# Optimization experiments

Hardware: AMD Instinct MI355X
Metric: run time of the kernel (lower is better)

Reference implementation:

```python
import jax, jax.numpy as jnp
import numpy as np

NUM_GRAPHS = 256
N_NODES = 100000
N_EDGES = 1200000
NODE_DIM = 64
NUM_LAYERS = 3
R_HID = 128
R_OUT = 32


def setup_inputs() -> dict:
    key = jax.random.key(0)
    ks = jax.random.split(key, 10)
    x = jax.random.normal(ks[0], (N_NODES, NODE_DIM), dtype=jnp.float32)
    src = jax.random.randint(ks[1], (N_EDGES,), 0, N_NODES)
    dst = jax.random.randint(ks[2], (N_EDGES,), 0, N_NODES)
    graph_ids = jnp.sort(jax.random.randint(ks[3], (N_NODES,), 0, NUM_GRAPHS))
    s = 1.0 / np.sqrt(NODE_DIM)
    gin_W = jax.random.normal(ks[4], (NUM_LAYERS, NODE_DIM, NODE_DIM), dtype=jnp.float32) * s
    gin_b = jnp.zeros((NUM_LAYERS, NODE_DIM), dtype=jnp.float32)
    eps = jnp.zeros((NUM_LAYERS,), dtype=jnp.float32)  # learnable GIN epsilon
    in_dim = NODE_DIM * NUM_LAYERS
    r_W1 = jax.random.normal(ks[5], (in_dim, R_HID), dtype=jnp.float32) / np.sqrt(in_dim)
    r_b1 = jnp.zeros((R_HID,), dtype=jnp.float32)
    r_W2 = jax.random.normal(ks[6], (R_HID, R_OUT), dtype=jnp.float32) / np.sqrt(R_HID)
    r_b2 = jnp.zeros((R_OUT,), dtype=jnp.float32)
    return {"x": x, "gin_W": gin_W, "gin_b": gin_b, "eps": eps,
            "r_W1": r_W1, "r_b1": r_b1, "r_W2": r_W2, "r_b2": r_b2,
            "src": src, "dst": dst, "graph_ids": graph_ids}


def reference(x, gin_W, gin_b, eps, r_W1, r_b1, r_W2, r_b2, src, dst, graph_ids):
    n = x.shape[0]
    h = x
    hs = []
    for l in range(NUM_LAYERS):  # fixed small layer loop
        # neighbor sum aggregation: scatter-add messages h[src] into dst
        agg = jax.ops.segment_sum(h[src], dst, num_segments=n)  # [N, D]
        h = jax.nn.relu(((1.0 + eps[l]) * h + agg) @ gin_W[l] + gin_b[l])
        hs.append(h)
    H = jnp.stack(hs, axis=1)  # [N, L, D]
    # dgl.sum_nodes per layer output == ragged segment-sum over graph ids
    g = jax.ops.segment_sum(H, graph_ids, num_segments=NUM_GRAPHS)  # [B, L, D]
    g = g.reshape(NUM_GRAPHS, -1)  # [B, L*D]
    # readout MLP (2 layers)
    out = jax.nn.relu(g @ r_W1 + r_b1) @ r_W2 + r_b2
    return out
```

## Files before the change

kernel.cpp:

```cpp
#include <hip/hip_runtime.h>


#define SPLIT 16
#define NBLK 512
#define BS 512

typedef unsigned short ushort_t;
typedef __bf16 v8bf __attribute__((ext_vector_type(8)));
typedef float v4f __attribute__((ext_vector_type(4)));

__device__ __forceinline__ float h2f_lo(unsigned int v) {
    return (float)__builtin_bit_cast(_Float16, (unsigned short)(v & 0xffffu));
}
__device__ __forceinline__ float h2f_hi(unsigned int v) {
    return (float)__builtin_bit_cast(_Float16, (unsigned short)(v >> 16));
}
__device__ __forceinline__ unsigned int f2h(float f) {
    return (unsigned int)__builtin_bit_cast(unsigned short, (_Float16)f);
}

__global__ __launch_bounds__(256) void pre_kernel(
        const int* __restrict__ dst, int* __restrict__ cnt2d,
        int E, int nbkt, int ebpb,
        const float* __restrict__ x, ushort_t* __restrict__ xh, int n4, int castBlocks,
        const float* __restrict__ W, ushort_t* __restrict__ whi,
        ushort_t* __restrict__ wlo, int wtotal) {
    __shared__ int lcnt[256];
    int t = threadIdx.x;
    int blk = blockIdx.x;
    if (blk < NBLK) {
        lcnt[t] = 0;
        __syncthreads();
        int base = blk * ebpb;
        int end = min(base + ebpb, E);
        for (int i = base + t; i < end; i += 256)
            atomicAdd(&lcnt[dst[i] >> 9], 1);
        __syncthreads();
        if (t < nbkt) cnt2d[(size_t)blk * nbkt + t] = lcnt[t];
    } else if (blk < NBLK + castBlocks) {
        int i = (blk - NBLK) * 256 + t;
        if (i < n4) {
            float4 v = ((const float4*)x)[i];
            uint2 p;
            p.x = f2h(v.x) | (f2h(v.y) << 16);
            p.y = f2h(v.z) | (f2h(v.w) << 16);
            ((uint2*)xh)[i] = p;
        }
    } else {
        int i = (blk - NBLK - castBlocks) * 256 + t;
        if (i < wtotal) {
            int l = i >> 12, r = i & 4095;
            int n = r >> 6, k = r & 63;
            float w = W[l * 4096 + k * 64 + n];
            __bf16 h = (__bf16)w;
            float rem = w - (float)h;
            whi[i] = __builtin_bit_cast(ushort_t, h);
            wlo[i] = __builtin_bit_cast(ushort_t, (__bf16)rem);
        }
    }
}

__global__ __launch_bounds__(256) void colscan_kernel(
        const int* __restrict__ cnt2d, int* __restrict__ blkoff,
        int* __restrict__ btot, int nbkt) {
    __shared__ int sh[256];
    int b = blockIdx.x, t = threadIdx.x;
    int i0 = 2 * t, i1 = 2 * t + 1;
    int v0 = cnt2d[(size_t)i0 * nbkt + b];
    int v1 = cnt2d[(size_t)i1 * nbkt + b];
    int pair = v0 + v1;
    sh[t] = pair;
    __syncthreads();
    for (int off = 1; off < 256; off <<= 1) {
        int u = (t >= off) ? sh[t - off] : 0;
        __syncthreads();
        sh[t] += u;
        __syncthreads();
    }
    int ex = sh[t] - pair;
    blkoff[(size_t)b * NBLK + i0] = ex;
    blkoff[(size_t)b * NBLK + i1] = ex + v0;
    if (t == 255) btot[b] = sh[255];
}

__global__ __launch_bounds__(256) void bucket_base_kernel(
        const int* __restrict__ btot, int* __restrict__ bbase,
        int* __restrict__ offsets, int nbkt, int N, int E) {
    __shared__ int sh[256];
    int t = threadIdx.x;
    int v = (t < nbkt) ? btot[t] : 0;
    sh[t] = v;
    __syncthreads();
    for (int off = 1; off < 256; off <<= 1) {
        int u = (t >= off) ? sh[t - off] : 0;
        __syncthreads();
        sh[t] += u;
        __syncthreads();
    }
    if (t < nbkt) bbase[t] = sh[t] - v;
    if (t == 0) { bbase[nbkt] = E; offsets[N] = E; }
}

__global__ __launch_bounds__(256) void bucket_scatter_kernel(
        const int* __restrict__ src, const int* __restrict__ dst,
        const int* __restrict__ bbase, const int* __restrict__ blkoff,
        unsigned int* __restrict__ bkt, int E, int nbkt, int ebpb) {
    __shared__ int lbase[256];
    __shared__ int lrank[256];
    int t = threadIdx.x;
    if (t < nbkt) lbase[t] = bbase[t] + blkoff[(size_t)t * NBLK + blockIdx.x];
    lrank[t] = 0;
    __syncthreads();
    int base = blockIdx.x * ebpb;
    int end = min(base + ebpb, E);
    for (int i = base + t; i < end; i += 256) {
        int d = dst[i];
        int b = d >> 9;
        int r = atomicAdd(&lrank[b], 1);
        bkt[lbase[b] + r] = ((unsigned int)src[i] << 9) | (unsigned int)(d & (BS - 1));
    }
}

__global__ __launch_bounds__(256) void csr_build_kernel(
        const unsigned int* __restrict__ bkt, const int* __restrict__ bbase,
        int* __restrict__ offsets, int* __restrict__ csr, int N, int nbkt) {
    __shared__ int cnt[BS];
    __shared__ int rank[BS];
    __shared__ int sh[256];
    int b = blockIdx.x, t = threadIdx.x;
    cnt[t] = 0; cnt[t + 256] = 0;
    rank[t] = 0; rank[t + 256] = 0;
    __syncthreads();
    int base = bbase[b], end = bbase[b + 1];
    for (int i = base + t; i < end; i += 256)
        atomicAdd(&cnt[bkt[i] & (BS - 1)], 1);
    __syncthreads();
    int i0 = 2 * t, i1 = 2 * t + 1;
    int v0 = cnt[i0], v1 = cnt[i1];
    int pair = v0 + v1;
    sh[t] = pair;
    __syncthreads();
    for (int off = 1; off < 256; off <<= 1) {
        int u = (t >= off) ? sh[t - off] : 0;
        __syncthreads();
        sh[t] += u;
        __syncthreads();
    }
    int ex = sh[t] - pair;
    __syncthreads();
    cnt[i0] = ex;
    cnt[i1] = ex + v0;
    __syncthreads();
    int d0 = (b << 9) + i0;
    if (d0 <= N) offsets[d0] = base + cnt[i0];
    int d1 = (b << 9) + i1;
    if (d1 <= N) offsets[d1] = base + cnt[i1];
    for (int i = base + t; i < end; i += 256) {
        unsigned int v = bkt[i];
        int dl = v & (BS - 1);
        int r = atomicAdd(&rank[dl], 1);
        csr[base + cnt[dl] + r] = (int)(v >> 9);
    }
}

__global__ __launch_bounds__(256) void layer_kernel(
        const ushort_t* __restrict__ hin, ushort_t* __restrict__ hout,
        const int* __restrict__ offsets, const int* __restrict__ csr,
        const ushort_t* __restrict__ wt_hi, const ushort_t* __restrict__ wt_lo,
        const float* __restrict__ gin_b, const float* __restrict__ eps_arr,
        int layer, int N) {
    __shared__ float rows[16 * 64];
    int t = threadIdx.x;
    int wv = t >> 6, lane = t & 63;
    int tile = blockIdx.x;
    float eps1 = 1.0f + eps_arr[layer];

    int nq = lane >> 4;
    int sl = lane & 15;
    int gbase = lane & 48;

    int node = tile * 16 + wv * 4 + nq;
    float ax = 0.f, ay = 0.f, az = 0.f, aw = 0.f;
    if (node < N) {
        int a = offsets[node], b = offsets[node + 1];
        int deg = b - a;
        int idxA = (sl < deg) ? csr[a + sl] : 0;
        int idxB = (16 + sl < deg) ? csr[a + 16 + sl] : 0;
        int d1 = min(deg, 16);
        #pragma unroll 8
        for (int j = 0; j < d1; ++j) {
            int s = __shfl(idxA, gbase + j, 64);
            uint2 v = ((const uint2*)(hin + (size_t)s * 64))[sl];
            ax += h2f_lo(v.x); ay += h2f_hi(v.x);
            az += h2f_lo(v.y); aw += h2f_hi(v.y);
        }
        int d2 = min(deg, 32);
        #pragma unroll 8
        for (int j = 16; j < d2; ++j) {
            int s = __shfl(idxB, gbase + (j - 16), 64);
            uint2 v = ((const uint2*)(hin + (size_t)s * 64))[sl];
            ax += h2f_lo(v.x); ay += h2f_hi(v.x);
            az += h2f_lo(v.y); aw += h2f_hi(v.y);
        }
        for (int e = a + 32; e < b; ++e) {
            int s = csr[e];
            uint2 v = ((const uint2*)(hin + (size_t)s * 64))[sl];
            ax += h2f_lo(v.x); ay += h2f_hi(v.x);
            az += h2f_lo(v.y); aw += h2f_hi(v.y);
        }
        uint2 self = ((const uint2*)(hin + (size_t)node * 64))[sl];
        ax = fmaf(eps1, h2f_lo(self.x), ax);
        ay = fmaf(eps1, h2f_hi(self.x), ay);
        az = fmaf(eps1, h2f_lo(self.y), az);
        aw = fmaf(eps1, h2f_hi(self.y), aw);
    }
    float4 r4; r4.x = ax; r4.y = ay; r4.z = az; r4.w = aw;
    *(float4*)&rows[(wv * 4 + nq) * 64 + sl * 4] = r4;
    __syncthreads();

    int c = lane & 15;
    int q = lane >> 4;
    int node16 = tile * 16 + c;
    int mt = wv;

    const ushort_t* Whi = wt_hi + layer * 4096;
    const ushort_t* Wlo = wt_lo + layer * 4096;
    const float*    bl  = gin_b + layer * 64;

    v8bf bhi[2], blo2[2];
    #pragma unroll
    for (int kt = 0; kt < 2; ++kt) {
        float4 f0 = *(float4*)&rows[c * 64 + kt * 32 + q * 8];
        float4 f1 = *(float4*)&rows[c * 64 + kt * 32 + q * 8 + 4];
        float xs[8] = {f0.x, f0.y, f0.z, f0.w, f1.x, f1.y, f1.z, f1.w};
        #pragma unroll
        for (int j = 0; j < 8; ++j) {
            __bf16 h = (__bf16)xs[j];
            bhi[kt][j] = h;
            blo2[kt][j] = (__bf16)(xs[j] - (float)h);
        }
    }

    v4f acc = {0.f, 0.f, 0.f, 0.f};
    #pragma unroll
    for (int kt = 0; kt < 2; ++kt) {
        int dim = mt * 16 + c;
        size_t off = (size_t)dim * 64 + kt * 32 + q * 8;
        v8bf ah = __builtin_bit_cast(v8bf, *(const uint4*)(Whi + off));
        v8bf al = __builtin_bit_cast(v8bf, *(const uint4*)(Wlo + off));
        acc = __builtin_amdgcn_mfma_f32_16x16x32_bf16(ah, bhi[kt],  acc, 0, 0, 0);
        acc = __builtin_amdgcn_mfma_f32_16x16x32_bf16(ah, blo2[kt], acc, 0, 0, 0);
        acc = __builtin_amdgcn_mfma_f32_16x16x32_bf16(al, bhi[kt],  acc, 0, 0, 0);
    }
    float4 bv = ((const float4*)(bl + mt * 16))[q];
    float o0 = fmaxf(acc[0] + bv.x, 0.f);
    float o1 = fmaxf(acc[1] + bv.y, 0.f);
    float o2 = fmaxf(acc[2] + bv.z, 0.f);
    float o3 = fmaxf(acc[3] + bv.w, 0.f);
    uint2 pk;
    pk.x = f2h(o0) | (f2h(o1) << 16);
    pk.y = f2h(o2) | (f2h(o3) << 16);
    if (node16 < N)
        *(uint2*)(hout + (size_t)node16 * 64 + mt * 16 + q * 4) = pk;
}

__global__ __launch_bounds__(192) void readout_part_kernel(
        const ushort_t* __restrict__ H, const int* __restrict__ gids,
        float* __restrict__ gpart, int N) {
    int graph = blockIdx.x / SPLIT;
    int sp    = blockIdx.x % SPLIT;
    int lo = 0, hi = N;
    while (lo < hi) { int mid = (lo + hi) >> 1; if (gids[mid] < graph) lo = mid + 1; else hi = mid; }
    int start = lo;
    int lo2 = start, hi2 = N;
    while (lo2 < hi2) { int mid = (lo2 + hi2) >> 1; if (gids[mid] < graph + 1) lo2 = mid + 1; else hi2 = mid; }
    int end = lo2;
    int t = threadIdx.x;
    int l = t >> 6, d = t & 63;
    float acc = 0.0f;
    int cnt = end - start;
    if (cnt > 0) {
        int per = (cnt + SPLIT - 1) / SPLIT;
        int cs = start + sp * per;
        int ce = min(cs + per, end);
        const ushort_t* Hl = H + (size_t)l * N * 64;
        for (int n = cs; n < ce; ++n)
            acc += (float)__builtin_bit_cast(_Float16, Hl[(size_t)n * 64 + d]);
    }
    gpart[(size_t)(graph * SPLIT + sp) * 192 + t] = acc;
}

__global__ __launch_bounds__(192) void mlp_kernel(
        const float* __restrict__ gpart,
        const float* __restrict__ W1, const float* __restrict__ b1,
        const float* __restrict__ W2, const float* __restrict__ b2,
        float* __restrict__ out) {
    __shared__ float gr[192];
    __shared__ float hid[128];
    int graph = blockIdx.x;
    int t = threadIdx.x;
    float a = 0.f;
    #pragma unroll
    for (int sp = 0; sp < SPLIT; ++sp)
        a += gpart[(size_t)(graph * SPLIT + sp) * 192 + t];
    gr[t] = a;
    __syncthreads();
    if (t < 128) {
        float s = b1[t];
        for (int k = 0; k < 192; ++k) s = fmaf(gr[k], W1[k * 128 + t], s);
        hid[t] = fmaxf(s, 0.0f);
    }
    __syncthreads();
    if (t < 32) {
        float s = b2[t];
        for (int k = 0; k < 128; ++k) s = fmaf(hid[k], W2[k * 32 + t], s);
        out[graph * 32 + t] = s;
    }
}

extern "C" void kernel_launch(void* const* d_in, const int* in_sizes, int n_in,
                              void* d_out, int out_size, void* d_ws, size_t ws_size,
                              hipStream_t stream) {
    const float* x     = (const float*)d_in[0];
    const float* gin_W = (const float*)d_in[1];
    const float* gin_b = (const float*)d_in[2];
    const float* eps   = (const float*)d_in[3];
    const float* r_W1  = (const float*)d_in[4];
    const float* r_b1  = (const float*)d_in[5];
    const float* r_W2  = (const float*)d_in[6];
    const float* r_b2  = (const float*)d_in[7];
    const int*   src   = (const int*)d_in[8];
    const int*   dst   = (const int*)d_in[9];
    const int*   gids  = (const int*)d_in[10];

    int N = in_sizes[0] / 64;
    int E = in_sizes[8];
    int B = out_size / 32;

    int nbkt = (N + BS - 1) / BS;
    int ebpb = (E + NBLK - 1) / NBLK;
    int n4 = N * 64 / 4;
    int castBlocks = (n4 + 255) / 256;
    int wtotal = 3 * 4096;
    int prepBlocks = (wtotal + 255) / 256;

    int* ws       = (int*)d_ws;
    float* gpart  = (float*)ws;
    int* cnt2d    = ws + (size_t)B * SPLIT * 192;
    int* blkoff   = cnt2d + (size_t)NBLK * nbkt;
    int* btot     = blkoff + (size_t)nbkt * NBLK;
    int* bbase    = btot + nbkt;
    int* offsets  = bbase + (nbkt + 1);
    unsigned int* bkt = (unsigned int*)(offsets + (N + 1));
    int* csr      = (int*)(bkt + E);
    size_t w      = (size_t)(csr + E - ws);
    w = (w + 15) & ~(size_t)15;
    ushort_t* xh  = (ushort_t*)(ws + w);
    ushort_t* H   = xh + (size_t)N * 64;
    ushort_t* whi = H + 3 * (size_t)N * 64;
    ushort_t* wlo = whi + 3 * 4096;

    pre_kernel<<<NBLK + castBlocks + prepBlocks, 256, 0, stream>>>(
        dst, cnt2d, E, nbkt, ebpb, x, xh, n4, castBlocks, gin_W, whi, wlo, wtotal);
    colscan_kernel<<<nbkt, 256, 0, stream>>>(cnt2d, blkoff, btot, nbkt);
    bucket_base_kernel<<<1, 256, 0, stream>>>(btot, bbase, offsets, nbkt, N, E);
    bucket_scatter_kernel<<<NBLK, 256, 0, stream>>>(src, dst, bbase, blkoff, bkt, E, nbkt, ebpb);
    csr_build_kernel<<<nbkt, 256, 0, stream>>>(bkt, bbase, offsets, csr, N, nbkt);

    int lbk = (N + 15) / 16;
    ushort_t* H0 = H;
    ushort_t* H1 = H + (size_t)N * 64;
    ushort_t* H2 = H + 2 * (size_t)N * 64;

    layer_kernel<<<lbk, 256, 0, stream>>>(xh, H0, offsets, csr, whi, wlo, gin_b, eps, 0, N);
    layer_kernel<<<lbk, 256, 0, stream>>>(H0, H1, offsets, csr, whi, wlo, gin_b, eps, 1, N);
    layer_kernel<<<lbk, 256, 0, stream>>>(H1, H2, offsets, csr, whi, wlo, gin_b, eps, 2, N);

    readout_part_kernel<<<B * SPLIT, 192, 0, stream>>>(H, gids, gpart, N);
    mlp_kernel<<<B, 192, 0, stream>>>(gpart, r_W1, r_b1, r_W2, r_b2, (float*)d_out);
}
```

Baseline: 334.0 us.

## Give each wave its own 16-node tile with edge-split gather and wave-local MFMA

Each wave now owns a 16-node tile. It processes the nodes one after another, spreading each node's edges across four lane groups and reducing the partial sums with cross-lane shuffles, then runs all four output MFMA tiles itself from wave-private shared memory. This removes the block-wide __syncthreads and balances gather work across lanes instead of one 16-lane group per node. The CSR index load for the next node is prefetched while the current node is gathered. The trade-off is a serial per-node loop inside each wave, extra shuffle reductions, and four times the weight loads and MFMAs per wave.

```diff
diff --git a/kernel.cpp b/kernel.cpp
--- a/kernel.cpp
+++ b/kernel.cpp
@@ -169,59 +169,67 @@
         const ushort_t* __restrict__ wt_hi, const ushort_t* __restrict__ wt_lo,
         const float* __restrict__ gin_b, const float* __restrict__ eps_arr,
         int layer, int N) {
-    __shared__ float rows[16 * 64];
+    __shared__ float rows[4 * 16 * 64];
     int t = threadIdx.x;
     int wv = t >> 6, lane = t & 63;
-    int tile = blockIdx.x;
+    int tile = blockIdx.x * 4 + wv;
+    if (tile * 16 >= N) return;
+    float* myrows = rows + wv * 16 * 64;
     float eps1 = 1.0f + eps_arr[layer];
 
-    int nq = lane >> 4;
+    int g  = lane >> 4;
     int sl = lane & 15;
-    int gbase = lane & 48;
-
-    int node = tile * 16 + wv * 4 + nq;
-    float ax = 0.f, ay = 0.f, az = 0.f, aw = 0.f;
-    if (node < N) {
-        int a = offsets[node], b = offsets[node + 1];
-        int deg = b - a;
-        int idxA = (sl < deg) ? csr[a + sl] : 0;
-        int idxB = (16 + sl < deg) ? csr[a + 16 + sl] : 0;
-        int d1 = min(deg, 16);
+
+    int off_l = offsets[min(tile * 16 + lane, N)];
+
+    int e0n = __shfl(off_l, 0, 64);
+    int degn = __shfl(off_l, 1, 64) - e0n;
+    int idxn = (lane < degn) ? csr[e0n + lane] : 0;
+
+    for (int k = 0; k < 16; ++k) {
+        int e0k = e0n, degk = degn, idxk = idxn;
+        if (k < 15) {
+            e0n = __shfl(off_l, k + 1, 64);
+            degn = __shfl(off_l, k + 2, 64) - e0n;
+            idxn = (lane < degn) ? csr[e0n + lane] : 0;
+        }
+        float ax = 0.f, ay = 0.f, az = 0.f, aw = 0.f;
+        int dcap = min(degk, 64);
         #pragma unroll 8
-        for (int j = 0; j < d1; ++j) {
-            int s = __shfl(idxA, gbase + j, 64);
+        for (int j = g; j < dcap; j += 4) {
+            int s = __shfl(idxk, j, 64);
             uint2 v = ((const uint2*)(hin + (size_t)s * 64))[sl];
             ax += h2f_lo(v.x); ay += h2f_hi(v.x);
             az += h2f_lo(v.y); aw += h2f_hi(v.y);
         }
-        int d2 = min(deg, 32);
-        #pragma unroll 8
-        for (int j = 16; j < d2; ++j) {
-            int s = __shfl(idxB, gbase + (j - 16), 64);
+        for (int j = 64 + g; j < degk; j += 4) {
+            int s = csr[e0k + j];
             uint2 v = ((const uint2*)(hin + (size_t)s * 64))[sl];
             ax += h2f_lo(v.x); ay += h2f_hi(v.x);
             az += h2f_lo(v.y); aw += h2f_hi(v.y);
         }
-        for (int e = a + 32; e < b; ++e) {
-            int s = csr[e];
-            uint2 v = ((const uint2*)(hin + (size_t)s * 64))[sl];
-            ax += h2f_lo(v.x); ay += h2f_hi(v.x);
-            az += h2f_lo(v.y); aw += h2f_hi(v.y);
-        }
-        uint2 self = ((const uint2*)(hin + (size_t)node * 64))[sl];
-        ax = fmaf(eps1, h2f_lo(self.x), ax);
-        ay = fmaf(eps1, h2f_hi(self.x), ay);
-        az = fmaf(eps1, h2f_lo(self.y), az);
-        aw = fmaf(eps1, h2f_hi(self.y), aw);
-    }
-    float4 r4; r4.x = ax; r4.y = ay; r4.z = az; r4.w = aw;
-    *(float4*)&rows[(wv * 4 + nq) * 64 + sl * 4] = r4;
-    __syncthreads();
+        ax += __shfl_xor(ax, 16, 64); ax += __shfl_xor(ax, 32, 64);
+        ay += __shfl_xor(ay, 16, 64); ay += __shfl_xor(ay, 32, 64);
+        az += __shfl_xor(az, 16, 64); az += __shfl_xor(az, 32, 64);
+        aw += __shfl_xor(aw, 16, 64); aw += __shfl_xor(aw, 32, 64);
+
+        int node = tile * 16 + k;
+        if (node < N) {
+            uint2 self = ((const uint2*)(hin + (size_t)node * 64))[sl];
+            ax = fmaf(eps1, h2f_lo(self.x), ax);
+            ay = fmaf(eps1, h2f_hi(self.x), ay);
+            az = fmaf(eps1, h2f_lo(self.y), az);
+            aw = fmaf(eps1, h2f_hi(self.y), aw);
+        }
+        if (g == 0) {
+            float4 r4; r4.x = ax; r4.y = ay; r4.z = az; r4.w = aw;
+            *(float4*)&myrows[k * 64 + sl * 4] = r4;
+        }
+    }
 
     int c = lane & 15;
     int q = lane >> 4;
     int node16 = tile * 16 + c;
-    int mt = wv;
 
     const ushort_t* Whi = wt_hi + layer * 4096;
     const ushort_t* Wlo = wt_lo + layer * 4096;
@@ -230,8 +238,8 @@
     v8bf bhi[2], blo2[2];
     #pragma unroll
     for (int kt = 0; kt < 2; ++kt) {
-        float4 f0 = *(float4*)&rows[c * 64 + kt * 32 + q * 8];
-        float4 f1 = *(float4*)&rows[c * 64 + kt * 32 + q * 8 + 4];
+        float4 f0 = *(float4*)&myrows[c * 64 + kt * 32 + q * 8];
+        float4 f1 = *(float4*)&myrows[c * 64 + kt * 32 + q * 8 + 4];
         float xs[8] = {f0.x, f0.y, f0.z, f0.w, f1.x, f1.y, f1.z, f1.w};
         #pragma unroll
         for (int j = 0; j < 8; ++j) {
@@ -241,27 +249,30 @@
         }
     }
 
-    v4f acc = {0.f, 0.f, 0.f, 0.f};
     #pragma unroll
-    for (int kt = 0; kt < 2; ++kt) {
-        int dim = mt * 16 + c;
-        size_t off = (size_t)dim * 64 + kt * 32 + q * 8;
-        v8bf ah = __builtin_bit_cast(v8bf, *(const uint4*)(Whi + off));
-        v8bf al = __builtin_bit_cast(v8bf, *(const uint4*)(Wlo + off));
-        acc = __builtin_amdgcn_mfma_f32_16x16x32_bf16(ah, bhi[kt],  acc, 0, 0, 0);
-        acc = __builtin_amdgcn_mfma_f32_16x16x32_bf16(ah, blo2[kt], acc, 0, 0, 0);
-        acc = __builtin_amdgcn_mfma_f32_16x16x32_bf16(al, bhi[kt],  acc, 0, 0, 0);
-    }
-    float4 bv = ((const float4*)(bl + mt * 16))[q];
-    float o0 = fmaxf(acc[0] + bv.x, 0.f);
-    float o1 = fmaxf(acc[1] + bv.y, 0.f);
-    float o2 = fmaxf(acc[2] + bv.z, 0.f);
-    float o3 = fmaxf(acc[3] + bv.w, 0.f);
-    uint2 pk;
-    pk.x = f2h(o0) | (f2h(o1) << 16);
-    pk.y = f2h(o2) | (f2h(o3) << 16);
-    if (node16 < N)
-        *(uint2*)(hout + (size_t)node16 * 64 + mt * 16 + q * 4) = pk;
+    for (int mt = 0; mt < 4; ++mt) {
+        v4f acc = {0.f, 0.f, 0.f, 0.f};
+        #pragma unroll
+        for (int kt = 0; kt < 2; ++kt) {
+            int dim = mt * 16 + c;
+            size_t off = (size_t)dim * 64 + kt * 32 + q * 8;
+            v8bf ah = __builtin_bit_cast(v8bf, *(const uint4*)(Whi + off));
+            v8bf al = __builtin_bit_cast(v8bf, *(const uint4*)(Wlo + off));
+            acc = __builtin_amdgcn_mfma_f32_16x16x32_bf16(ah, bhi[kt],  acc, 0, 0, 0);
+            acc = __builtin_amdgcn_mfma_f32_16x16x32_bf16(ah, blo2[kt], acc, 0, 0, 0);
+            acc = __builtin_amdgcn_mfma_f32_16x16x32_bf16(al, bhi[kt],  acc, 0, 0, 0);
+        }
+        float4 bv = ((const float4*)(bl + mt * 16))[q];
+        float o0 = fmaxf(acc[0] + bv.x, 0.f);
+        float o1 = fmaxf(acc[1] + bv.y, 0.f);
+        float o2 = fmaxf(acc[2] + bv.z, 0.f);
+        float o3 = fmaxf(acc[3] + bv.w, 0.f);
+        uint2 pk;
+        pk.x = f2h(o0) | (f2h(o1) << 16);
+        pk.y = f2h(o2) | (f2h(o3) << 16);
+        if (node16 < N)
+            *(uint2*)(hout + (size_t)node16 * 64 + mt * 16 + q * 4) = pk;
+    }
 }
 
 __global__ __launch_bounds__(192) void readout_part_kernel(
@@ -367,7 +378,7 @@
     bucket_scatter_kernel<<<NBLK, 256, 0, stream>>>(src, dst, bbase, blkoff, bkt, E, nbkt, ebpb);
     csr_build_kernel<<<nbkt, 256, 0, stream>>>(bkt, bbase, offsets, csr, N, nbkt);
 
-    int lbk = (N + 15) / 16;
+    int lbk = (N + 63) / 64;
     ushort_t* H0 = H;
     ushort_t* H1 = H + (size_t)N * 64;
     ushort_t* H2 = H + 2 * (size_t)N * 64;
```

Measured after the change: 323.3 us. 1.03x faster.
